# Performance work log

Measured on AMD Instinct MI355X. Metric: run time of the kernel, lower is better.

Reference implementation:

```python
import jax, jax.numpy as jnp
import numpy as np

B, N, D, H = 4, 2048, 1024, 16
DH = D // H


def setup_inputs() -> dict:
    key = jax.random.key(0)
    ks = jax.random.split(key, 9)
    s = 1.0 / np.sqrt(D)
    return {
        "x": jax.random.normal(ks[0], (B, N, D), dtype=jnp.float32),
        "Wq": jax.random.normal(ks[1], (D, D), dtype=jnp.float32) * s,
        "bq": jax.random.normal(ks[2], (D,), dtype=jnp.float32) * 0.01,
        "Wk": jax.random.normal(ks[3], (D, D), dtype=jnp.float32) * s,
        "bk": jax.random.normal(ks[4], (D,), dtype=jnp.float32) * 0.01,
        "Wv": jax.random.normal(ks[5], (D, D), dtype=jnp.float32) * s,
        "bv": jax.random.normal(ks[6], (D,), dtype=jnp.float32) * 0.01,
        "Wp": jax.random.normal(ks[7], (D, D), dtype=jnp.float32) * s,
        "bp": jax.random.normal(ks[8], (D,), dtype=jnp.float32) * 0.01,
    }


def reference(x, Wq, bq, Wk, bk, Wv, bv, Wp, bp):
    b, n, d = x.shape
    # torch Linear: x @ W.T + b; reshape to (b, h, n, dh)
    def heads(W, bias):
        y = jnp.einsum('bnd,ed->bne', x, W) + bias
        return y.reshape(b, n, H, DH).transpose(0, 2, 1, 3)
    q, k, v = heads(Wq, bq), heads(Wk, bk), heads(Wv, bv)
    # NOTE: source multiplies by sqrt(d_head) (bug in original), kept faithfully
    scale = jnp.sqrt(jnp.float32(DH))
    att = jnp.einsum('bhqd,bhkd->bhqk', q, k) * scale
    causal = jnp.triu(jnp.ones((n, n), dtype=bool), k=1)  # True above diagonal
    att = jnp.where(causal, -jnp.inf, att)
    att = jax.nn.softmax(att, axis=-1)
    # dropout is eval-mode identity
    out = jnp.einsum('bhqk,bhkd->bhqd', att, v)
    out = out.transpose(0, 2, 1, 3).reshape(b, n, d)
    return jnp.einsum('bnd,ed->bne', out, Wp) + bp
```

## Files before the change

kernel.cpp:

```cpp
#include <hip/hip_runtime.h>
#include <hip/hip_fp16.h>


typedef _Float16 half8 __attribute__((ext_vector_type(8)));
typedef _Float16 half4 __attribute__((ext_vector_type(4)));
typedef float f32x4 __attribute__((ext_vector_type(4)));
typedef unsigned int u32x4 __attribute__((ext_vector_type(4)));

#define DEV __device__ __forceinline__
#define MFMA16(a, b, c) __builtin_amdgcn_mfma_f32_16x16x32_f16(a, b, c, 0, 0, 0)

DEV void gload_lds16(const void* g, void* l) {
  __builtin_amdgcn_global_load_lds(
      (const __attribute__((address_space(1))) void*)g,
      (__attribute__((address_space(3))) void*)l, 16, 0, 0);
}

__global__ __launch_bounds__(256) void cast_f32h(const float* __restrict__ s,
                                                 __half* __restrict__ d, int n8) {
  int i = blockIdx.x * 256 + threadIdx.x;
  if (i >= n8) return;
  const float4* sp = (const float4*)s + (size_t)i * 2;
  float4 a = sp[0], b = sp[1];
  half8 h;
  h[0] = (_Float16)a.x; h[1] = (_Float16)a.y; h[2] = (_Float16)a.z; h[3] = (_Float16)a.w;
  h[4] = (_Float16)b.x; h[5] = (_Float16)b.y; h[6] = (_Float16)b.z; h[7] = (_Float16)b.w;
  *((half8*)d + i) = h;
}

template <int MODE>
__global__ __launch_bounds__(256) void gemm128(
    const __half* __restrict__ A, const __half* __restrict__ Bm,
    const float* __restrict__ b0, const float* __restrict__ b1,
    const float* __restrict__ b2, __half* __restrict__ oh,
    __half* __restrict__ vtp, float* __restrict__ of) {
  const int m0 = blockIdx.y * 128;
  const int n0 = blockIdx.x * 128;
  const int tid = threadIdx.x;
  const int w = tid >> 6, lane = tid & 63;
  const int lr = lane & 15, lq = lane >> 4;
  const int wr = w >> 1, wc = w & 1;

  __shared__ alignas(16) __half As[128 * 64];
  __shared__ alignas(16) __half Bs[128 * 64];

  f32x4 acc[4][4] = {};

  const int arow = lane >> 3;
  const int acol = (lane & 7) * 8;
  const __half* Agp = A + ((size_t)m0 + w * 32 + arow) * 1024 + acol;
  const __half* Bgp = Bm + ((size_t)n0 + w * 32 + arow) * 1024 + acol;

  for (int kt = 0; kt < 16; ++kt) {
#pragma unroll
    for (int j = 0; j < 4; ++j) {
      gload_lds16(Agp + j * 8192 + kt * 64, As + (w * 4 + j) * 512);
      gload_lds16(Bgp + j * 8192 + kt * 64, Bs + (w * 4 + j) * 512);
    }
    __syncthreads();
#pragma unroll
    for (int s = 0; s < 2; ++s) {
      half8 af[4], bf[4];
#pragma unroll
      for (int i = 0; i < 4; ++i) {
        af[i] = *(const half8*)(As + (wr * 64 + i * 16 + lr) * 64 + s * 32 + lq * 8);
        bf[i] = *(const half8*)(Bs + (wc * 64 + i * 16 + lr) * 64 + s * 32 + lq * 8);
      }
#pragma unroll
      for (int mi = 0; mi < 4; ++mi)
#pragma unroll
        for (int ni = 0; ni < 4; ++ni)
          acc[mi][ni] = MFMA16(af[mi], bf[ni], acc[mi][ni]);
    }
    __syncthreads();
  }

  if (MODE == 0) {
#pragma unroll
    for (int ni = 0; ni < 4; ++ni) {
      int col = n0 + wc * 64 + ni * 16 + lr;
      int t = col >> 10, e = col & 1023;
      const float* bb = (t == 0) ? b0 : ((t == 1) ? b1 : b2);
      float bias = bb[e];
      int hh = e >> 6, dh = e & 63;
      if (t == 2) {
#pragma unroll
        for (int mi = 0; mi < 4; ++mi) {
          int row = m0 + wr * 64 + mi * 16 + lq * 4;
          int b_ = row >> 11, n = row & 2047;
          half4 h;
#pragma unroll
          for (int r = 0; r < 4; ++r) h[r] = (_Float16)(acc[mi][ni][r] + bias);
          *(half4*)(vtp + (size_t)(b_ * 16 + hh) * 131072 + (size_t)dh * 2048 + n) = h;
        }
      } else {
        float scale = (t == 0) ? 11.541560327111707f : 1.0f;
        __half* base = oh + (size_t)t * 8388608 + dh;
#pragma unroll
        for (int mi = 0; mi < 4; ++mi)
#pragma unroll
          for (int r = 0; r < 4; ++r) {
            int row = m0 + wr * 64 + mi * 16 + lq * 4 + r;
            int b_ = row >> 11, n = row & 2047;
            float v = (acc[mi][ni][r] + bias) * scale;
            base[(((size_t)(b_ * 16 + hh) * 2048 + n) * 64)] = __float2half(v);
          }
      }
    }
  } else {
#pragma unroll
    for (int ni = 0; ni < 4; ++ni) {
      int col = n0 + wc * 64 + ni * 16 + lr;
      float bias = b0[col];
#pragma unroll
      for (int mi = 0; mi < 4; ++mi)
#pragma unroll
        for (int r = 0; r < 4; ++r) {
          int row = m0 + wr * 64 + mi * 16 + lq * 4 + r;
          of[(size_t)row * 1024 + col] = acc[mi][ni][r] + bias;
        }
    }
  }
}

__global__ __launch_bounds__(512, 4) void attn128(const __half* __restrict__ Q,
                                                  const __half* __restrict__ K,
                                                  const __half* __restrict__ Vt,
                                                  __half* __restrict__ O) {
  const int wg = blockIdx.x;
  const int bh = wg & 63;
  const int pair = wg >> 6;
  const int b = bh >> 4, h = bh & 15;
  const int tid = threadIdx.x;
  const int w = tid >> 6, lane = tid & 63;
  const int lr = lane & 15, lq = lane >> 4;
  const int hi = lane >> 5;
  const int sA = (lane & 15) | ((lane & 16) << 1);
  const int sB = sA + 16;

  __shared__ alignas(16) __half Ks[2][4096];
  __shared__ alignas(16) __half Vs[2][4096];

  const __half* Kb = K + (size_t)bh * 131072;
  const __half* Vb = Vt + (size_t)bh * 131072;

  const int srow = lane >> 3;
  const int scol = ((lane & 7) ^ srow) * 8;

  for (int half_ = 0; half_ < 2; ++half_) {
    const int qt = half_ ? (15 - pair) : pair;
    const int q0 = qt * 128;
    const int ktend = 2 * qt + 2;
    const int rmin = q0 + w * 16;
    const int myq = rmin + lr;

    const __half* Qp = Q + ((size_t)bh * 2048 + q0 + w * 16) * 64;
    half8 qf0 = *(const half8*)(Qp + lr * 64 + lq * 8);
    half8 qf1 = *(const half8*)(Qp + lr * 64 + 32 + lq * 8);

    f32x4 oacc[4] = {};
    float m = -INFINITY, l = 0.f;

    gload_lds16(Kb + (size_t)(0 + w * 8 + srow) * 64 + scol, Ks[0] + w * 512);
    gload_lds16(Vb + (size_t)(w * 8 + srow) * 2048 + 0 + scol, Vs[0] + w * 512);
    asm volatile("" ::: "memory");

    for (int kt = 0; kt < ktend; ++kt) {
      const int cur = kt & 1;
      const int k0 = kt * 64;
      if (kt + 1 < ktend) {
        const int kn = k0 + 64;
        gload_lds16(Kb + (size_t)(kn + w * 8 + srow) * 64 + scol,
                    Ks[cur ^ 1] + w * 512);
        gload_lds16(Vb + (size_t)(w * 8 + srow) * 2048 + kn + scol,
                    Vs[cur ^ 1] + w * 512);
        asm volatile("s_waitcnt vmcnt(2)" ::: "memory");
      } else {
        asm volatile("s_waitcnt vmcnt(0)" ::: "memory");
      }
      __builtin_amdgcn_s_barrier();
      asm volatile("" ::: "memory");

      const char* Kc = (const char*)Ks[cur];
      const char* Vc = (const char*)Vs[cur];
      const bool active = (k0 <= rmin + 15);
      if (active) {
        f32x4 sacc[4] = {};
        __builtin_amdgcn_s_setprio(1);
#pragma unroll
        for (int nt = 0; nt < 4; ++nt) {
          int row = nt * 16 + lr;
          half8 kb0 = *(const half8*)(Kc + ((row * 128 + lq * 16) ^ ((row & 7) << 4)));
          half8 kb1 = *(const half8*)(Kc + ((row * 128 + 64 + lq * 16) ^ ((row & 7) << 4)));
          sacc[nt] = MFMA16(kb0, qf0, sacc[nt]);
          sacc[nt] = MFMA16(kb1, qf1, sacc[nt]);
        }
        __builtin_amdgcn_s_setprio(0);

        if (k0 + 63 > rmin) {
#pragma unroll
          for (int nt = 0; nt < 4; ++nt)
#pragma unroll
            for (int r = 0; r < 4; ++r) {
              int key = k0 + nt * 16 + lq * 4 + r;
              if (key > myq) sacc[nt][r] = -INFINITY;
            }
        }

        float rm = fmaxf(fmaxf(fmaxf(sacc[0][0], sacc[0][1]),
                               fmaxf(sacc[0][2], sacc[0][3])),
                         fmaxf(fmaxf(sacc[1][0], sacc[1][1]),
                               fmaxf(sacc[1][2], sacc[1][3])));
        rm = fmaxf(rm, fmaxf(fmaxf(fmaxf(sacc[2][0], sacc[2][1]),
                                   fmaxf(sacc[2][2], sacc[2][3])),
                             fmaxf(fmaxf(sacc[3][0], sacc[3][1]),
                                   fmaxf(sacc[3][2], sacc[3][3]))));
        rm = fmaxf(rm, __shfl_xor(rm, 16));
        rm = fmaxf(rm, __shfl_xor(rm, 32));

        if (__any(rm > m + 8.f)) {
          float mn = fmaxf(m, rm);
          float al = __builtin_amdgcn_exp2f(m - mn);
          m = mn;
          l *= al;
          float al4[4];
#pragma unroll
          for (int r = 0; r < 4; ++r) al4[r] = __shfl(al, lq * 4 + r);
#pragma unroll
          for (int dt = 0; dt < 4; ++dt)
#pragma unroll
            for (int r = 0; r < 4; ++r) oacc[dt][r] *= al4[r];
        }

        float ps = 0.f;
#pragma unroll
        for (int nt = 0; nt < 4; ++nt) {
          float p0 = __builtin_amdgcn_exp2f(sacc[nt][0] - m);
          float p1 = __builtin_amdgcn_exp2f(sacc[nt][1] - m);
          float p2 = __builtin_amdgcn_exp2f(sacc[nt][2] - m);
          float p3 = __builtin_amdgcn_exp2f(sacc[nt][3] - m);
          sacc[nt][0] = p0; sacc[nt][1] = p1;
          sacc[nt][2] = p2; sacc[nt][3] = p3;
          ps += (p0 + p1) + (p2 + p3);
        }
        ps += __shfl_xor(ps, 16);
        ps += __shfl_xor(ps, 32);
        l += ps;

        unsigned ph[8];
#pragma unroll
        for (int nt = 0; nt < 4; ++nt) {
          __half2 a = __floats2half2_rn(sacc[nt][0], sacc[nt][1]);
          __half2 bq_ = __floats2half2_rn(sacc[nt][2], sacc[nt][3]);
          ph[2 * nt] = *(unsigned*)&a;
          ph[2 * nt + 1] = *(unsigned*)&bq_;
        }

        u32x4 fa, fb;
        {
          unsigned t0, t1;
          t0 = __shfl((int)ph[0], sA); t1 = __shfl((int)ph[2], sA);
          fa[0] = hi ? t1 : t0;
          t0 = __shfl((int)ph[1], sA); t1 = __shfl((int)ph[3], sA);
          fa[1] = hi ? t1 : t0;
          t0 = __shfl((int)ph[0], sB); t1 = __shfl((int)ph[2], sB);
          fa[2] = hi ? t1 : t0;
          t0 = __shfl((int)ph[1], sB); t1 = __shfl((int)ph[3], sB);
          fa[3] = hi ? t1 : t0;
          t0 = __shfl((int)ph[4], sA); t1 = __shfl((int)ph[6], sA);
          fb[0] = hi ? t1 : t0;
          t0 = __shfl((int)ph[5], sA); t1 = __shfl((int)ph[7], sA);
          fb[1] = hi ? t1 : t0;
          t0 = __shfl((int)ph[4], sB); t1 = __shfl((int)ph[6], sB);
          fb[2] = hi ? t1 : t0;
          t0 = __shfl((int)ph[5], sB); t1 = __shfl((int)ph[7], sB);
          fb[3] = hi ? t1 : t0;
        }
        half8 pa0 = *(half8*)&fa;
        half8 pa1 = *(half8*)&fb;

        __builtin_amdgcn_s_setprio(1);
#pragma unroll
        for (int dt = 0; dt < 4; ++dt) {
          int row = dt * 16 + lr;
          half8 vb0 = *(const half8*)(Vc + ((row * 128 + lq * 16) ^ ((row & 7) << 4)));
          half8 vb1 = *(const half8*)(Vc + ((row * 128 + 64 + lq * 16) ^ ((row & 7) << 4)));
          oacc[dt] = MFMA16(pa0, vb0, oacc[dt]);
          oacc[dt] = MFMA16(pa1, vb1, oacc[dt]);
        }
        __builtin_amdgcn_s_setprio(0);
      }
      asm volatile("s_waitcnt lgkmcnt(0)" ::: "memory");
      __builtin_amdgcn_s_barrier();
      asm volatile("" ::: "memory");
    }

    float linv = 1.0f / l;
    float inv4[4];
#pragma unroll
    for (int r = 0; r < 4; ++r) inv4[r] = __shfl(linv, lq * 4 + r);
    __half* Op = O + ((size_t)b * 2048 + q0 + w * 16) * 1024 + h * 64;
#pragma unroll
    for (int dt = 0; dt < 4; ++dt)
#pragma unroll
      for (int r = 0; r < 4; ++r)
        Op[(size_t)(lq * 4 + r) * 1024 + dt * 16 + lr] =
            __float2half(oacc[dt][r] * inv4[r]);
  }
}

extern "C" void kernel_launch(void* const* d_in, const int* in_sizes, int n_in,
                              void* d_out, int out_size, void* d_ws,
                              size_t ws_size, hipStream_t stream) {
  const float* x = (const float*)d_in[0];
  const float* Wq = (const float*)d_in[1];
  const float* bq = (const float*)d_in[2];
  const float* Wk = (const float*)d_in[3];
  const float* bk = (const float*)d_in[4];
  const float* Wv = (const float*)d_in[5];
  const float* bv = (const float*)d_in[6];
  const float* Wp = (const float*)d_in[7];
  const float* bp = (const float*)d_in[8];

  char* ws = (char*)d_ws;
  const size_t XB = 0;
  const size_t WQKV = XB + 16777216;
  const size_t WPB = WQKV + 6291456;
  const size_t QKV = WPB + 2097152;
  const size_t VT = QKV + 50331648;
  const size_t OB = VT + 16777216;

  __half* xb = (__half*)(ws + XB);
  __half* wqkv = (__half*)(ws + WQKV);
  __half* wpb = (__half*)(ws + WPB);
  __half* qkv = (__half*)(ws + QKV);
  __half* vt = (__half*)(ws + VT);
  __half* ob = (__half*)(ws + OB);

  cast_f32h<<<4096, 256, 0, stream>>>(x, xb, 1048576);
  cast_f32h<<<512, 256, 0, stream>>>(Wq, wqkv, 131072);
  cast_f32h<<<512, 256, 0, stream>>>(Wk, wqkv + 1048576, 131072);
  cast_f32h<<<512, 256, 0, stream>>>(Wv, wqkv + 2097152, 131072);
  cast_f32h<<<512, 256, 0, stream>>>(Wp, wpb, 131072);

  gemm128<0><<<dim3(24, 64), 256, 0, stream>>>(xb, wqkv, bq, bk, bv, qkv, vt,
                                               nullptr);
  attn128<<<dim3(512), 512, 0, stream>>>(qkv, qkv + 8388608, vt, ob);
  gemm128<1><<<dim3(8, 64), 256, 0, stream>>>(ob, wpb, bp, nullptr, nullptr,
                                              nullptr, nullptr, (float*)d_out);
}
```

Baseline: 191.2 us.

## Fuse cast kernels into one launch and split attention to one q-tile per block

Merges the five fp32-to-fp16 cast launches into a single kernel that routes each thread to x or one of the four weight matrices. The attention kernel no longer pairs a short and a long causal query tile per workgroup. It launches 1024 workgroups, each handling one 128-row query tile, scheduled longest-first (qt = 15 - wg>>6). This cuts launch overhead and exposes more parallelism, but it gives up the built-in load balancing of pairing and relies on the hardware scheduler to fill the tail with short tiles.

```diff
diff --git a/kernel.cpp b/kernel.cpp
--- a/kernel.cpp
+++ b/kernel.cpp
@@ -16,16 +16,30 @@
       (__attribute__((address_space(3))) void*)l, 16, 0, 0);
 }
 
-__global__ __launch_bounds__(256) void cast_f32h(const float* __restrict__ s,
-                                                 __half* __restrict__ d, int n8) {
+__global__ __launch_bounds__(256) void cast_all(
+    const float* __restrict__ x, const float* __restrict__ Wq,
+    const float* __restrict__ Wk, const float* __restrict__ Wv,
+    const float* __restrict__ Wp, __half* __restrict__ xb,
+    __half* __restrict__ wqkv, __half* __restrict__ wpb) {
   int i = blockIdx.x * 256 + threadIdx.x;
-  if (i >= n8) return;
-  const float4* sp = (const float4*)s + (size_t)i * 2;
+  const float* s;
+  __half* d;
+  int j;
+  if (i < 1048576) {
+    s = x; d = xb; j = i;
+  } else {
+    int k = i - 1048576;
+    int sel = k >> 17;
+    j = k & 131071;
+    s = (sel == 0) ? Wq : (sel == 1) ? Wk : (sel == 2) ? Wv : Wp;
+    d = (sel == 3) ? wpb : (wqkv + sel * 1048576);
+  }
+  const float4* sp = (const float4*)s + (size_t)j * 2;
   float4 a = sp[0], b = sp[1];
   half8 h;
   h[0] = (_Float16)a.x; h[1] = (_Float16)a.y; h[2] = (_Float16)a.z; h[3] = (_Float16)a.w;
   h[4] = (_Float16)b.x; h[5] = (_Float16)b.y; h[6] = (_Float16)b.z; h[7] = (_Float16)b.w;
-  *((half8*)d + i) = h;
+  *((half8*)d + j) = h;
 }
 
 template <int MODE>
@@ -129,7 +143,7 @@
                                                   __half* __restrict__ O) {
   const int wg = blockIdx.x;
   const int bh = wg & 63;
-  const int pair = wg >> 6;
+  const int qt = 15 - (wg >> 6);
   const int b = bh >> 4, h = bh & 15;
   const int tid = threadIdx.x;
   const int w = tid >> 6, lane = tid & 63;
@@ -147,166 +161,163 @@
   const int srow = lane >> 3;
   const int scol = ((lane & 7) ^ srow) * 8;
 
-  for (int half_ = 0; half_ < 2; ++half_) {
-    const int qt = half_ ? (15 - pair) : pair;
-    const int q0 = qt * 128;
-    const int ktend = 2 * qt + 2;
-    const int rmin = q0 + w * 16;
-    const int myq = rmin + lr;
-
-    const __half* Qp = Q + ((size_t)bh * 2048 + q0 + w * 16) * 64;
-    half8 qf0 = *(const half8*)(Qp + lr * 64 + lq * 8);
-    half8 qf1 = *(const half8*)(Qp + lr * 64 + 32 + lq * 8);
-
-    f32x4 oacc[4] = {};
-    float m = -INFINITY, l = 0.f;
-
-    gload_lds16(Kb + (size_t)(0 + w * 8 + srow) * 64 + scol, Ks[0] + w * 512);
-    gload_lds16(Vb + (size_t)(w * 8 + srow) * 2048 + 0 + scol, Vs[0] + w * 512);
+  const int q0 = qt * 128;
+  const int ktend = 2 * qt + 2;
+  const int rmin = q0 + w * 16;
+  const int myq = rmin + lr;
+
+  const __half* Qp = Q + ((size_t)bh * 2048 + q0 + w * 16) * 64;
+  half8 qf0 = *(const half8*)(Qp + lr * 64 + lq * 8);
+  half8 qf1 = *(const half8*)(Qp + lr * 64 + 32 + lq * 8);
+
+  f32x4 oacc[4] = {};
+  float m = -INFINITY, l = 0.f;
+
+  gload_lds16(Kb + (size_t)(0 + w * 8 + srow) * 64 + scol, Ks[0] + w * 512);
+  gload_lds16(Vb + (size_t)(w * 8 + srow) * 2048 + 0 + scol, Vs[0] + w * 512);
+  asm volatile("" ::: "memory");
+
+  for (int kt = 0; kt < ktend; ++kt) {
+    const int cur = kt & 1;
+    const int k0 = kt * 64;
+    if (kt + 1 < ktend) {
+      const int kn = k0 + 64;
+      gload_lds16(Kb + (size_t)(kn + w * 8 + srow) * 64 + scol,
+                  Ks[cur ^ 1] + w * 512);
+      gload_lds16(Vb + (size_t)(w * 8 + srow) * 2048 + kn + scol,
+                  Vs[cur ^ 1] + w * 512);
+      asm volatile("s_waitcnt vmcnt(2)" ::: "memory");
+    } else {
+      asm volatile("s_waitcnt vmcnt(0)" ::: "memory");
+    }
+    __builtin_amdgcn_s_barrier();
     asm volatile("" ::: "memory");
 
-    for (int kt = 0; kt < ktend; ++kt) {
-      const int cur = kt & 1;
-      const int k0 = kt * 64;
-      if (kt + 1 < ktend) {
-        const int kn = k0 + 64;
-        gload_lds16(Kb + (size_t)(kn + w * 8 + srow) * 64 + scol,
-                    Ks[cur ^ 1] + w * 512);
-        gload_lds16(Vb + (size_t)(w * 8 + srow) * 2048 + kn + scol,
-                    Vs[cur ^ 1] + w * 512);
-        asm volatile("s_waitcnt vmcnt(2)" ::: "memory");
-      } else {
-        asm volatile("s_waitcnt vmcnt(0)" ::: "memory");
-      }
-      __builtin_amdgcn_s_barrier();
-      asm volatile("" ::: "memory");
-
-      const char* Kc = (const char*)Ks[cur];
-      const char* Vc = (const char*)Vs[cur];
-      const bool active = (k0 <= rmin + 15);
-      if (active) {
-        f32x4 sacc[4] = {};
-        __builtin_amdgcn_s_setprio(1);
-#pragma unroll
-        for (int nt = 0; nt < 4; ++nt) {
-          int row = nt * 16 + lr;
-          half8 kb0 = *(const half8*)(Kc + ((row * 128 + lq * 16) ^ ((row & 7) << 4)));
-          half8 kb1 = *(const half8*)(Kc + ((row * 128 + 64 + lq * 16) ^ ((row & 7) << 4)));
-          sacc[nt] = MFMA16(kb0, qf0, sacc[nt]);
-          sacc[nt] = MFMA16(kb1, qf1, sacc[nt]);
-        }
-        __builtin_amdgcn_s_setprio(0);
-
-        if (k0 + 63 > rmin) {
-#pragma unroll
-          for (int nt = 0; nt < 4; ++nt)
-#pragma unroll
-            for (int r = 0; r < 4; ++r) {
-              int key = k0 + nt * 16 + lq * 4 + r;
-              if (key > myq) sacc[nt][r] = -INFINITY;
-            }
-        }
-
-        float rm = fmaxf(fmaxf(fmaxf(sacc[0][0], sacc[0][1]),
-                               fmaxf(sacc[0][2], sacc[0][3])),
-                         fmaxf(fmaxf(sacc[1][0], sacc[1][1]),
-                               fmaxf(sacc[1][2], sacc[1][3])));
-        rm = fmaxf(rm, fmaxf(fmaxf(fmaxf(sacc[2][0], sacc[2][1]),
-                                   fmaxf(sacc[2][2], sacc[2][3])),
-                             fmaxf(fmaxf(sacc[3][0], sacc[3][1]),
-                                   fmaxf(sacc[3][2], sacc[3][3]))));
-        rm = fmaxf(rm, __shfl_xor(rm, 16));
-        rm = fmaxf(rm, __shfl_xor(rm, 32));
-
-        if (__any(rm > m + 8.f)) {
-          float mn = fmaxf(m, rm);
-          float al = __builtin_amdgcn_exp2f(m - mn);
-          m = mn;
-          l *= al;
-          float al4[4];
-#pragma unroll
-          for (int r = 0; r < 4; ++r) al4[r] = __shfl(al, lq * 4 + r);
-#pragma unroll
-          for (int dt = 0; dt < 4; ++dt)
-#pragma unroll
-            for (int r = 0; r < 4; ++r) oacc[dt][r] *= al4[r];
-        }
-
-        float ps = 0.f;
-#pragma unroll
-        for (int nt = 0; nt < 4; ++nt) {
-          float p0 = __builtin_amdgcn_exp2f(sacc[nt][0] - m);
-          float p1 = __builtin_amdgcn_exp2f(sacc[nt][1] - m);
-          float p2 = __builtin_amdgcn_exp2f(sacc[nt][2] - m);
-          float p3 = __builtin_amdgcn_exp2f(sacc[nt][3] - m);
-          sacc[nt][0] = p0; sacc[nt][1] = p1;
-          sacc[nt][2] = p2; sacc[nt][3] = p3;
-          ps += (p0 + p1) + (p2 + p3);
-        }
-        ps += __shfl_xor(ps, 16);
-        ps += __shfl_xor(ps, 32);
-        l += ps;
-
-        unsigned ph[8];
-#pragma unroll
-        for (int nt = 0; nt < 4; ++nt) {
-          __half2 a = __floats2half2_rn(sacc[nt][0], sacc[nt][1]);
-          __half2 bq_ = __floats2half2_rn(sacc[nt][2], sacc[nt][3]);
-          ph[2 * nt] = *(unsigned*)&a;
-          ph[2 * nt + 1] = *(unsigned*)&bq_;
-        }
-
-        u32x4 fa, fb;
-        {
-          unsigned t0, t1;
-          t0 = __shfl((int)ph[0], sA); t1 = __shfl((int)ph[2], sA);
-          fa[0] = hi ? t1 : t0;
-          t0 = __shfl((int)ph[1], sA); t1 = __shfl((int)ph[3], sA);
-          fa[1] = hi ? t1 : t0;
-          t0 = __shfl((int)ph[0], sB); t1 = __shfl((int)ph[2], sB);
-          fa[2] = hi ? t1 : t0;
-          t0 = __shfl((int)ph[1], sB); t1 = __shfl((int)ph[3], sB);
-          fa[3] = hi ? t1 : t0;
-          t0 = __shfl((int)ph[4], sA); t1 = __shfl((int)ph[6], sA);
-          fb[0] = hi ? t1 : t0;
-          t0 = __shfl((int)ph[5], sA); t1 = __shfl((int)ph[7], sA);
-          fb[1] = hi ? t1 : t0;
-          t0 = __shfl((int)ph[4], sB); t1 = __shfl((int)ph[6], sB);
-          fb[2] = hi ? t1 : t0;
-          t0 = __shfl((int)ph[5], sB); t1 = __shfl((int)ph[7], sB);
-          fb[3] = hi ? t1 : t0;
-        }
-        half8 pa0 = *(half8*)&fa;
-        half8 pa1 = *(half8*)&fb;
-
-        __builtin_amdgcn_s_setprio(1);
-#pragma unroll
-        for (int dt = 0; dt < 4; ++dt) {
-          int row = dt * 16 + lr;
-          half8 vb0 = *(const half8*)(Vc + ((row * 128 + lq * 16) ^ ((row & 7) << 4)));
-          half8 vb1 = *(const half8*)(Vc + ((row * 128 + 64 + lq * 16) ^ ((row & 7) << 4)));
-          oacc[dt] = MFMA16(pa0, vb0, oacc[dt]);
-          oacc[dt] = MFMA16(pa1, vb1, oacc[dt]);
-        }
-        __builtin_amdgcn_s_setprio(0);
-      }
-      asm volatile("s_waitcnt lgkmcnt(0)" ::: "memory");
-      __builtin_amdgcn_s_barrier();
-      asm volatile("" ::: "memory");
-    }
-
-    float linv = 1.0f / l;
-    float inv4[4];
-#pragma unroll
-    for (int r = 0; r < 4; ++r) inv4[r] = __shfl(linv, lq * 4 + r);
-    __half* Op = O + ((size_t)b * 2048 + q0 + w * 16) * 1024 + h * 64;
-#pragma unroll
-    for (int dt = 0; dt < 4; ++dt)
-#pragma unroll
-      for (int r = 0; r < 4; ++r)
-        Op[(size_t)(lq * 4 + r) * 1024 + dt * 16 + lr] =
-            __float2half(oacc[dt][r] * inv4[r]);
+    const char* Kc = (const char*)Ks[cur];
+    const char* Vc = (const char*)Vs[cur];
+    const bool active = (k0 <= rmin + 15);
+    if (active) {
+      f32x4 sacc[4] = {};
+      __builtin_amdgcn_s_setprio(1);
+#pragma unroll
+      for (int nt = 0; nt < 4; ++nt) {
+        int row = nt * 16 + lr;
+        half8 kb0 = *(const half8*)(Kc + ((row * 128 + lq * 16) ^ ((row & 7) << 4)));
+        half8 kb1 = *(const half8*)(Kc + ((row * 128 + 64 + lq * 16) ^ ((row & 7) << 4)));
+        sacc[nt] = MFMA16(kb0, qf0, sacc[nt]);
+        sacc[nt] = MFMA16(kb1, qf1, sacc[nt]);
+      }
+      __builtin_amdgcn_s_setprio(0);
+
+      if (k0 + 63 > rmin) {
+#pragma unroll
+        for (int nt = 0; nt < 4; ++nt)
+#pragma unroll
+          for (int r = 0; r < 4; ++r) {
+            int key = k0 + nt * 16 + lq * 4 + r;
+            if (key > myq) sacc[nt][r] = -INFINITY;
+          }
+      }
+
+      float rm = fmaxf(fmaxf(fmaxf(sacc[0][0], sacc[0][1]),
+                             fmaxf(sacc[0][2], sacc[0][3])),
+                       fmaxf(fmaxf(sacc[1][0], sacc[1][1]),
+                             fmaxf(sacc[1][2], sacc[1][3])));
+      rm = fmaxf(rm, fmaxf(fmaxf(fmaxf(sacc[2][0], sacc[2][1]),
+                                 fmaxf(sacc[2][2], sacc[2][3])),
+                           fmaxf(fmaxf(sacc[3][0], sacc[3][1]),
+                                 fmaxf(sacc[3][2], sacc[3][3]))));
+      rm = fmaxf(rm, __shfl_xor(rm, 16));
+      rm = fmaxf(rm, __shfl_xor(rm, 32));
+
+      if (__any(rm > m + 8.f)) {
+        float mn = fmaxf(m, rm);
+        float al = __builtin_amdgcn_exp2f(m - mn);
+        m = mn;
+        l *= al;
+        float al4[4];
+#pragma unroll
+        for (int r = 0; r < 4; ++r) al4[r] = __shfl(al, lq * 4 + r);
+#pragma unroll
+        for (int dt = 0; dt < 4; ++dt)
+#pragma unroll
+          for (int r = 0; r < 4; ++r) oacc[dt][r] *= al4[r];
+      }
+
+      float ps = 0.f;
+#pragma unroll
+      for (int nt = 0; nt < 4; ++nt) {
+        float p0 = __builtin_amdgcn_exp2f(sacc[nt][0] - m);
+        float p1 = __builtin_amdgcn_exp2f(sacc[nt][1] - m);
+        float p2 = __builtin_amdgcn_exp2f(sacc[nt][2] - m);
+        float p3 = __builtin_amdgcn_exp2f(sacc[nt][3] - m);
+        sacc[nt][0] = p0; sacc[nt][1] = p1;
+        sacc[nt][2] = p2; sacc[nt][3] = p3;
+        ps += (p0 + p1) + (p2 + p3);
+      }
+      ps += __shfl_xor(ps, 16);
+      ps += __shfl_xor(ps, 32);
+      l += ps;
+
+      unsigned ph[8];
+#pragma unroll
+      for (int nt = 0; nt < 4; ++nt) {
+        __half2 a = __floats2half2_rn(sacc[nt][0], sacc[nt][1]);
+        __half2 bq_ = __floats2half2_rn(sacc[nt][2], sacc[nt][3]);
+        ph[2 * nt] = *(unsigned*)&a;
+        ph[2 * nt + 1] = *(unsigned*)&bq_;
+      }
+
+      u32x4 fa, fb;
+      {
+        unsigned t0, t1;
+        t0 = __shfl((int)ph[0], sA); t1 = __shfl((int)ph[2], sA);
+        fa[0] = hi ? t1 : t0;
+        t0 = __shfl((int)ph[1], sA); t1 = __shfl((int)ph[3], sA);
+        fa[1] = hi ? t1 : t0;
+        t0 = __shfl((int)ph[0], sB); t1 = __shfl((int)ph[2], sB);
+        fa[2] = hi ? t1 : t0;
+        t0 = __shfl((int)ph[1], sB); t1 = __shfl((int)ph[3], sB);
+        fa[3] = hi ? t1 : t0;
+        t0 = __shfl((int)ph[4], sA); t1 = __shfl((int)ph[6], sA);
+        fb[0] = hi ? t1 : t0;
+        t0 = __shfl((int)ph[5], sA); t1 = __shfl((int)ph[7], sA);
+        fb[1] = hi ? t1 : t0;
+        t0 = __shfl((int)ph[4], sB); t1 = __shfl((int)ph[6], sB);
+        fb[2] = hi ? t1 : t0;
+        t0 = __shfl((int)ph[5], sB); t1 = __shfl((int)ph[7], sB);
+        fb[3] = hi ? t1 : t0;
+      }
+      half8 pa0 = *(half8*)&fa;
+      half8 pa1 = *(half8*)&fb;
+
+      __builtin_amdgcn_s_setprio(1);
+#pragma unroll
+      for (int dt = 0; dt < 4; ++dt) {
+        int row = dt * 16 + lr;
+        half8 vb0 = *(const half8*)(Vc + ((row * 128 + lq * 16) ^ ((row & 7) << 4)));
+        half8 vb1 = *(const half8*)(Vc + ((row * 128 + 64 + lq * 16) ^ ((row & 7) << 4)));
+        oacc[dt] = MFMA16(pa0, vb0, oacc[dt]);
+        oacc[dt] = MFMA16(pa1, vb1, oacc[dt]);
+      }
+      __builtin_amdgcn_s_setprio(0);
+    }
+    asm volatile("s_waitcnt lgkmcnt(0)" ::: "memory");
+    __builtin_amdgcn_s_barrier();
+    asm volatile("" ::: "memory");
   }
+
+  float linv = 1.0f / l;
+  float inv4[4];
+#pragma unroll
+  for (int r = 0; r < 4; ++r) inv4[r] = __shfl(linv, lq * 4 + r);
+  __half* Op = O + ((size_t)b * 2048 + q0 + w * 16) * 1024 + h * 64;
+#pragma unroll
+  for (int dt = 0; dt < 4; ++dt)
+#pragma unroll
+    for (int r = 0; r < 4; ++r)
+      Op[(size_t)(lq * 4 + r) * 1024 + dt * 16 + lr] =
+          __float2half(oacc[dt][r] * inv4[r]);
 }
 
 extern "C" void kernel_launch(void* const* d_in, const int* in_sizes, int n_in,
@@ -337,15 +348,11 @@
   __half* vt = (__half*)(ws + VT);
   __half* ob = (__half*)(ws + OB);
 
-  cast_f32h<<<4096, 256, 0, stream>>>(x, xb, 1048576);
-  cast_f32h<<<512, 256, 0, stream>>>(Wq, wqkv, 131072);
-  cast_f32h<<<512, 256, 0, stream>>>(Wk, wqkv + 1048576, 131072);
-  cast_f32h<<<512, 256, 0, stream>>>(Wv, wqkv + 2097152, 131072);
-  cast_f32h<<<512, 256, 0, stream>>>(Wp, wpb, 131072);
+  cast_all<<<6144, 256, 0, stream>>>(x, Wq, Wk, Wv, Wp, xb, wqkv, wpb);
 
   gemm128<0><<<dim3(24, 64), 256, 0, stream>>>(xb, wqkv, bq, bk, bv, qkv, vt,
                                                nullptr);
-  attn128<<<dim3(512), 512, 0, stream>>>(qkv, qkv + 8388608, vt, ob);
+  attn128<<<dim3(1024), 512, 0, stream>>>(qkv, qkv + 8388608, vt, ob);
   gemm128<1><<<dim3(8, 64), 256, 0, stream>>>(ob, wpb, bp, nullptr, nullptr,
                                               nullptr, nullptr, (float*)d_out);
 }
```

New measurement: 184.4 us. 1.04x faster.
